# Performance work log

Hardware: AMD Instinct MI355X
Metric: run time of the kernel (lower is better)

Reference implementation:

```python
import jax, jax.numpy as jnp
import numpy as np

NUM_FEATURES = 128
NUM_FILTERS = 128

def setup_inputs() -> dict:
    key = jax.random.key(0)
    k1, k2, k3, k4, k5 = jax.random.split(key, 5)
    B, N, F = 4, 2048, NUM_FEATURES
    x = jax.random.normal(k1, (B, N, F), dtype=jnp.float32)
    A = jax.random.normal(k2, (B, N, N), dtype=jnp.float32)
    # Conv1D(num_filters, kernel_size=1, use_bias=False) == per-node linear F -> filters
    W = jax.random.normal(k3, (F, NUM_FILTERS), dtype=jnp.float32) * (1.0 / np.sqrt(F))
    # self.a: Conv1D(1, kernel_size=1) with bias == linear filters -> 1 (shared for x_i and x_j)
    a_w = jax.random.normal(k4, (NUM_FILTERS, 1), dtype=jnp.float32) * (1.0 / np.sqrt(NUM_FILTERS))
    a_b = jax.random.normal(k5, (1,), dtype=jnp.float32) * 0.01
    bias = jnp.zeros((NUM_FILTERS,), dtype=jnp.float32)
    return {"x": x, "A": A, "W": W, "a_w": a_w, "a_b": a_b, "bias": bias}

def reference(x, A, W, a_w, a_b, bias):
    # project features: [B,N,F] @ [F,Ff] -> [B,N,Ff]
    h = jnp.einsum('bnf,fg->bng', x, W)
    # shared attention projection (x_i and x_j use the same layer): [B,N,1]
    s = jnp.einsum('bng,go->bno', h, a_w) + a_b
    # additive scores s_i + s_j^T -> [B,N,N]
    e = s + jnp.swapaxes(s, 1, 2)
    e = jnp.where(e >= 0, e, 0.2 * e)  # LeakyReLU(0.2)
    attn = jax.nn.softmax(e + A, axis=-1)
    out = jnp.einsum('bij,bjg->big', attn, h) + bias
    return out
```

## Files before the change

kernel.cpp:

```cpp
#include <hip/hip_runtime.h>
#include <hip/hip_bf16.h>
#include <stdint.h>

#define BB 4
#define NN 2048
#define FF 128

typedef __attribute__((ext_vector_type(8))) short bf16x8;
typedef __attribute__((ext_vector_type(4))) float f32x4;

__device__ inline unsigned pk_bf16(float a, float b) {
    union { float f; unsigned u; } x, y;
    x.f = a; y.f = b;
    unsigned xu = x.u + (0x7fffu + ((x.u >> 16) & 1u));
    unsigned yu = y.u + (0x7fffu + ((y.u >> 16) & 1u));
    return (xu >> 16) | (yu & 0xffff0000u);
}

#define XT_P 136
#define WT_P 136

__global__ __launch_bounds__(256) void k1_proj(
    const float* __restrict__ x, const float* __restrict__ W,
    const float* __restrict__ a_w, const float* __restrict__ a_b,
    uint16_t* __restrict__ Ht, float* __restrict__ s_out)
{
    __shared__ uint16_t xt[16 * XT_P];
    __shared__ uint16_t Wt[128 * WT_P];
    __shared__ float sredw[4 * 16];

    const int t = threadIdx.x;
    const int w = t >> 6, l = t & 63;
    const int m16 = l & 15, q = l >> 4;
    const int b = blockIdx.x >> 7;
    const int n0 = (blockIdx.x & 127) << 4;

    const int c4 = (t & 31) * 4, kh = (t >> 5) * 16;
    float4 wr0[8], wr1[8];
    #pragma unroll
    for (int kk = 0; kk < 8; ++kk) {
        const int k = kh + 2 * kk;
        wr0[kk] = *(const float4*)(W + (size_t)k * 128 + c4);
        wr1[kk] = *(const float4*)(W + (size_t)(k + 1) * 128 + c4);
    }
    {
        const int row = t >> 4, c0 = (t & 15) * 8;
        const float* xr = x + ((size_t)(b * NN + n0 + row)) * FF + c0;
        const float4 v0 = *(const float4*)xr;
        const float4 v1 = *(const float4*)(xr + 4);
        unsigned* dst = (unsigned*)(xt + row * XT_P + c0);
        dst[0] = pk_bf16(v0.x, v0.y); dst[1] = pk_bf16(v0.z, v0.w);
        dst[2] = pk_bf16(v1.x, v1.y); dst[3] = pk_bf16(v1.z, v1.w);
    }
    #pragma unroll
    for (int kk = 0; kk < 8; ++kk) {
        const int k = kh + 2 * kk;
        *(unsigned*)(Wt + (c4 + 0) * WT_P + k) = pk_bf16(wr0[kk].x, wr1[kk].x);
        *(unsigned*)(Wt + (c4 + 1) * WT_P + k) = pk_bf16(wr0[kk].y, wr1[kk].y);
        *(unsigned*)(Wt + (c4 + 2) * WT_P + k) = pk_bf16(wr0[kk].z, wr1[kk].z);
        *(unsigned*)(Wt + (c4 + 3) * WT_P + k) = pk_bf16(wr0[kk].w, wr1[kk].w);
    }
    const int g0 = (2 * w) * 16 + m16, g1 = (2 * w + 1) * 16 + m16;
    const float aw0 = a_w[g0], aw1 = a_w[g1];
    __syncthreads();

    f32x4 acc0 = {}, acc1 = {};
    bf16x8 af[4];
    #pragma unroll
    for (int dk = 0; dk < 4; ++dk)
        af[dk] = *(const bf16x8*)(xt + m16 * XT_P + dk * 32 + q * 8);
    #pragma unroll
    for (int dk = 0; dk < 4; ++dk) {
        bf16x8 b0 = *(const bf16x8*)(Wt + g0 * WT_P + dk * 32 + q * 8);
        bf16x8 b1 = *(const bf16x8*)(Wt + g1 * WT_P + dk * 32 + q * 8);
        acc0 = __builtin_amdgcn_mfma_f32_16x16x32_bf16(af[dk], b0, acc0, 0, 0, 0);
        acc1 = __builtin_amdgcn_mfma_f32_16x16x32_bf16(af[dk], b1, acc1, 0, 0, 0);
    }

    float sp[4];
    #pragma unroll
    for (int r = 0; r < 4; ++r) sp[r] = acc0[r] * aw0 + acc1[r] * aw1;
    #pragma unroll
    for (int off = 1; off < 16; off <<= 1)
        #pragma unroll
        for (int r = 0; r < 4; ++r) sp[r] += __shfl_xor(sp[r], off, 64);
    if (m16 == 0) {
        #pragma unroll
        for (int r = 0; r < 4; ++r) sredw[w * 16 + q * 4 + r] = sp[r];
    }
    {
        uint2 o0 = { pk_bf16(acc0[0], acc0[1]), pk_bf16(acc0[2], acc0[3]) };
        uint2 o1 = { pk_bf16(acc1[0], acc1[1]), pk_bf16(acc1[2], acc1[3]) };
        *(uint2*)(Ht + ((size_t)(b * 128 + g0)) * NN + n0 + q * 4) = o0;
        *(uint2*)(Ht + ((size_t)(b * 128 + g1)) * NN + n0 + q * 4) = o1;
    }
    __syncthreads();
    if (t < 16)
        s_out[b * NN + n0 + t] = sredw[t] + sredw[16 + t] + sredw[32 + t] + sredw[48 + t] + a_b[0];
}

#define JS 8
#define IRND 8
#define P_RW 132
#define O_RW 36

__global__ __launch_bounds__(256, 2) void k2_attn(
    const float* __restrict__ A, const uint16_t* __restrict__ Ht,
    const float* __restrict__ s, uint16_t* __restrict__ po,
    float* __restrict__ prs)
{
    __shared__ unsigned Pbuf[2][16 * P_RW];
    __shared__ float    Osc[4][16 * O_RW];
    __shared__ float    rsw[2][4][16];

    const int t = threadIdx.x;
    const int w = t >> 6, l = t & 63;
    const int m16 = l & 15, q = l >> 4;

    const int bx = blockIdx.x;
    const int b  = bx & 3;
    const int js = (bx >> 2) & 7;
    const int is = bx >> 5;
    const int j0 = js * 256;
    const int ibase = is * 128;

    const float* sb = s + b * NN;
    const float* Ab = A + (size_t)b * NN * NN;
    const uint16_t* Hb = Ht + (size_t)b * FF * NN;

    const int jc0 = j0 + w * 32 + q * 8;
    const int jc1 = j0 + (w + 4) * 32 + q * 8;

    float4 sj00 = *(const float4*)(sb + jc0);
    float4 sj01 = *(const float4*)(sb + jc0 + 4);
    float4 sj10 = *(const float4*)(sb + jc1);
    float4 sj11 = *(const float4*)(sb + jc1 + 4);

    bf16x8 hf0[8], hf1[8];
    #pragma unroll
    for (int ks = 0; ks < 8; ++ks) {
        const int jj = j0 + ks * 32 + q * 8;
        hf0[ks] = *(const bf16x8*)(Hb + (size_t)(w * 32 + m16) * NN + jj);
        hf1[ks] = *(const bf16x8*)(Hb + (size_t)(w * 32 + 16 + m16) * NN + jj);
    }

    const float* Ar = Ab + (size_t)(ibase + m16) * NN;
    float4 a00 = *(const float4*)(Ar + jc0);
    float4 a01 = *(const float4*)(Ar + jc0 + 4);
    float4 a10 = *(const float4*)(Ar + jc1);
    float4 a11 = *(const float4*)(Ar + jc1 + 4);
    float si = sb[ibase + m16];

    const size_t slice = (size_t)(js * BB + b);

    #pragma unroll
    for (int r = 0; r < IRND; ++r) {
        const int i0r = ibase + r * 16;
        const int i0n = ibase + ((r + 1) & (IRND - 1)) * 16;
        const int par = r & 1;

        const float* An = Ab + (size_t)(i0n + m16) * NN;
        float4 n00 = *(const float4*)(An + jc0);
        float4 n01 = *(const float4*)(An + jc0 + 4);
        float4 n10 = *(const float4*)(An + jc1);
        float4 n11 = *(const float4*)(An + jc1 + 4);
        const float sin_ = sb[i0n + m16];

        const float svv[16] = {sj00.x,sj00.y,sj00.z,sj00.w, sj01.x,sj01.y,sj01.z,sj01.w,
                               sj10.x,sj10.y,sj10.z,sj10.w, sj11.x,sj11.y,sj11.z,sj11.w};
        const float avv[16] = {a00.x,a00.y,a00.z,a00.w, a01.x,a01.y,a01.z,a01.w,
                               a10.x,a10.y,a10.z,a10.w, a11.x,a11.y,a11.z,a11.w};
        float pv[16]; float rs = 0.f;
        #pragma unroll
        for (int j = 0; j < 16; ++j) {
            float e = si + svv[j];
            e = fmaxf(e, 0.2f * e);
            pv[j] = __expf(e + avv[j]);
            rs += pv[j];
        }
        union { unsigned u[4]; uint4 v4; } fa0, fa1;
        #pragma unroll
        for (int j = 0; j < 4; ++j) {
            fa0.u[j] = pk_bf16(pv[2 * j], pv[2 * j + 1]);
            fa1.u[j] = pk_bf16(pv[8 + 2 * j], pv[9 + 2 * j]);
        }
        *(uint4*)&Pbuf[par][m16 * P_RW + (w * 4 + q) * 4]        = fa0.v4;
        *(uint4*)&Pbuf[par][m16 * P_RW + (w * 4 + q + 16) * 4]   = fa1.v4;

        rs += __shfl_xor(rs, 16, 64);
        rs += __shfl_xor(rs, 32, 64);
        if (q == 0) rsw[par][w][m16] = rs;

        asm volatile("s_waitcnt lgkmcnt(0)\n\ts_barrier" ::: "memory");

        bf16x8 pa[8];
        #pragma unroll
        for (int ks = 0; ks < 8; ++ks)
            pa[ks] = *(const bf16x8*)&Pbuf[par][m16 * P_RW + ks * 16 + q * 4];

        f32x4 acc0 = {0.f, 0.f, 0.f, 0.f}, acc1 = {0.f, 0.f, 0.f, 0.f};
        #pragma unroll
        for (int ks = 0; ks < 8; ++ks) {
            acc0 = __builtin_amdgcn_mfma_f32_16x16x32_bf16(pa[ks], hf0[ks], acc0, 0, 0, 0);
            acc1 = __builtin_amdgcn_mfma_f32_16x16x32_bf16(pa[ks], hf1[ks], acc1, 0, 0, 0);
        }

        #pragma unroll
        for (int rr = 0; rr < 4; ++rr) {
            Osc[w][(q * 4 + rr) * O_RW + m16]      = acc0[rr];
            Osc[w][(q * 4 + rr) * O_RW + 16 + m16] = acc1[rr];
        }
        {
            const int row = l >> 2, c0 = (l & 3) * 8;
            const float4 u0 = *(const float4*)&Osc[w][row * O_RW + c0];
            const float4 u1 = *(const float4*)&Osc[w][row * O_RW + c0 + 4];
            uint4 ov = { pk_bf16(u0.x, u0.y), pk_bf16(u0.z, u0.w),
                         pk_bf16(u1.x, u1.y), pk_bf16(u1.z, u1.w) };
            *(uint4*)(po + ((slice * NN + i0r + row) * FF + w * 32 + c0)) = ov;
            if (t < 16)
                prs[slice * NN + i0r + t] = rsw[par][0][t] + rsw[par][1][t]
                                          + rsw[par][2][t] + rsw[par][3][t];
        }

        a00 = n00; a01 = n01; a10 = n10; a11 = n11; si = sin_;
    }
}

__global__ __launch_bounds__(256) void k3_red(
    const uint16_t* __restrict__ po, const float* __restrict__ prs,
    const float* __restrict__ bias, float* __restrict__ out)
{
    const int gid = blockIdx.x * 256 + threadIdx.x;
    const int g8 = (gid & 15) * 8;
    const int i = (gid >> 4) & (NN - 1);
    const int b = gid >> 15;

    float v[8] = {0.f,0.f,0.f,0.f,0.f,0.f,0.f,0.f};
    float rsum = 0.f;
    #pragma unroll
    for (int js = 0; js < JS; ++js) {
        const size_t base = (size_t)(js * BB + b) * NN + i;
        const uint4 pv_ = *(const uint4*)(po + base * FF + g8);
        const unsigned uu[4] = {pv_.x, pv_.y, pv_.z, pv_.w};
        #pragma unroll
        for (int k = 0; k < 4; ++k) {
            union { unsigned u; float f; } lo, hi;
            lo.u = uu[k] << 16;
            hi.u = uu[k] & 0xffff0000u;
            v[2 * k]     += lo.f;
            v[2 * k + 1] += hi.f;
        }
        rsum += prs[base];
    }
    const float inv = 1.0f / rsum;
    const float4 b0 = *(const float4*)(bias + g8);
    const float4 b1 = *(const float4*)(bias + g8 + 4);
    float4 o0 = { v[0]*inv + b0.x, v[1]*inv + b0.y, v[2]*inv + b0.z, v[3]*inv + b0.w };
    float4 o1 = { v[4]*inv + b1.x, v[5]*inv + b1.y, v[6]*inv + b1.z, v[7]*inv + b1.w };
    float* op = out + ((size_t)(b * NN + i)) * FF + g8;
    *(float4*)op = o0;
    *(float4*)(op + 4) = o1;
}

extern "C" void kernel_launch(void* const* d_in, const int* in_sizes, int n_in,
                              void* d_out, int out_size, void* d_ws, size_t ws_size,
                              hipStream_t stream) {
    const float* x    = (const float*)d_in[0];
    const float* A    = (const float*)d_in[1];
    const float* W    = (const float*)d_in[2];
    const float* a_w  = (const float*)d_in[3];
    const float* a_b  = (const float*)d_in[4];
    const float* bias = (const float*)d_in[5];
    float* out = (float*)d_out;

    char* ws = (char*)d_ws;
    uint16_t* Ht = (uint16_t*)ws;
    float* s = (float*)(ws + 2 * 1024 * 1024);
    uint16_t* po = (uint16_t*)(ws + 2 * 1024 * 1024 + 65536);
    float* prs = (float*)(ws + 2 * 1024 * 1024 + 65536 + (size_t)JS * BB * NN * FF * 2);

    k1_proj<<<BB * (NN / 16), 256, 0, stream>>>(x, W, a_w, a_b, Ht, s);
    k2_attn<<<JS * 16 * BB, 256, 0, stream>>>(A, Ht, s, po, prs);
    k3_red<<<(BB * NN * FF) / (256 * 8), 256, 0, stream>>>(po, prs, bias, out);
}
```

Baseline: 120.3 us.

## Compute attention probabilities per wave in registers, dropping LDS exchange and barrier

Each wave now computes exp-scores for its 16 rows across all 256 j columns itself and feeds them straight into the MFMA A operand. This removes the shared-memory P buffer, the per-round barrier and the cross-wave row-sum exchange. In exchange every wave loads the full A tile and s vector and repeats the exp work, about four times the per-block A load traffic and transcendental work. It also holds 64 more registers for the prefetched A fragments, and the round loop is no longer fully unrolled.

New measurement: 145.8 us. 21.2% more time.

```diff
diff --git a/kernel.cpp b/kernel.cpp
--- a/kernel.cpp
+++ b/kernel.cpp
@@ -101,7 +101,6 @@
 
 #define JS 8
 #define IRND 8
-#define P_RW 132
 #define O_RW 36
 
 __global__ __launch_bounds__(256, 2) void k2_attn(
@@ -109,9 +108,7 @@
     const float* __restrict__ s, uint16_t* __restrict__ po,
     float* __restrict__ prs)
 {
-    __shared__ unsigned Pbuf[2][16 * P_RW];
-    __shared__ float    Osc[4][16 * O_RW];
-    __shared__ float    rsw[2][4][16];
+    __shared__ float Osc[4][16 * O_RW];
 
     const int t = threadIdx.x;
     const int w = t >> 6, l = t & 63;
@@ -128,14 +125,6 @@
     const float* Ab = A + (size_t)b * NN * NN;
     const uint16_t* Hb = Ht + (size_t)b * FF * NN;
 
-    const int jc0 = j0 + w * 32 + q * 8;
-    const int jc1 = j0 + (w + 4) * 32 + q * 8;
-
-    float4 sj00 = *(const float4*)(sb + jc0);
-    float4 sj01 = *(const float4*)(sb + jc0 + 4);
-    float4 sj10 = *(const float4*)(sb + jc1);
-    float4 sj11 = *(const float4*)(sb + jc1 + 4);
-
     bf16x8 hf0[8], hf1[8];
     #pragma unroll
     for (int ks = 0; ks < 8; ++ks) {
@@ -144,66 +133,59 @@
         hf1[ks] = *(const bf16x8*)(Hb + (size_t)(w * 32 + 16 + m16) * NN + jj);
     }
 
-    const float* Ar = Ab + (size_t)(ibase + m16) * NN;
-    float4 a00 = *(const float4*)(Ar + jc0);
-    float4 a01 = *(const float4*)(Ar + jc0 + 4);
-    float4 a10 = *(const float4*)(Ar + jc1);
-    float4 a11 = *(const float4*)(Ar + jc1 + 4);
-    float si = sb[ibase + m16];
+    const float* sjp = sb + j0 + q * 8;
+
+    float4 af[16];
+    {
+        const float* Ar0 = Ab + (size_t)(ibase + m16) * NN + j0 + q * 8;
+        #pragma unroll
+        for (int ks = 0; ks < 8; ++ks) {
+            af[2 * ks]     = *(const float4*)(Ar0 + ks * 32);
+            af[2 * ks + 1] = *(const float4*)(Ar0 + ks * 32 + 4);
+        }
+    }
 
     const size_t slice = (size_t)(js * BB + b);
 
-    #pragma unroll
     for (int r = 0; r < IRND; ++r) {
         const int i0r = ibase + r * 16;
         const int i0n = ibase + ((r + 1) & (IRND - 1)) * 16;
-        const int par = r & 1;
-
-        const float* An = Ab + (size_t)(i0n + m16) * NN;
-        float4 n00 = *(const float4*)(An + jc0);
-        float4 n01 = *(const float4*)(An + jc0 + 4);
-        float4 n10 = *(const float4*)(An + jc1);
-        float4 n11 = *(const float4*)(An + jc1 + 4);
-        const float sin_ = sb[i0n + m16];
-
-        const float svv[16] = {sj00.x,sj00.y,sj00.z,sj00.w, sj01.x,sj01.y,sj01.z,sj01.w,
-                               sj10.x,sj10.y,sj10.z,sj10.w, sj11.x,sj11.y,sj11.z,sj11.w};
-        const float avv[16] = {a00.x,a00.y,a00.z,a00.w, a01.x,a01.y,a01.z,a01.w,
-                               a10.x,a10.y,a10.z,a10.w, a11.x,a11.y,a11.z,a11.w};
-        float pv[16]; float rs = 0.f;
-        #pragma unroll
-        for (int j = 0; j < 16; ++j) {
-            float e = si + svv[j];
-            e = fmaxf(e, 0.2f * e);
-            pv[j] = __expf(e + avv[j]);
-            rs += pv[j];
-        }
-        union { unsigned u[4]; uint4 v4; } fa0, fa1;
-        #pragma unroll
-        for (int j = 0; j < 4; ++j) {
-            fa0.u[j] = pk_bf16(pv[2 * j], pv[2 * j + 1]);
-            fa1.u[j] = pk_bf16(pv[8 + 2 * j], pv[9 + 2 * j]);
-        }
-        *(uint4*)&Pbuf[par][m16 * P_RW + (w * 4 + q) * 4]        = fa0.v4;
-        *(uint4*)&Pbuf[par][m16 * P_RW + (w * 4 + q + 16) * 4]   = fa1.v4;
+        const float* An = Ab + (size_t)(i0n + m16) * NN + j0 + q * 8;
+        const float si = sb[i0r + m16];
+
+        f32x4 acc0 = {0.f, 0.f, 0.f, 0.f}, acc1 = {0.f, 0.f, 0.f, 0.f};
+        float rs = 0.f;
+
+        #pragma unroll
+        for (int ks = 0; ks < 8; ++ks) {
+            const float4 a0 = af[2 * ks], a1 = af[2 * ks + 1];
+            af[2 * ks]     = *(const float4*)(An + ks * 32);
+            af[2 * ks + 1] = *(const float4*)(An + ks * 32 + 4);
+            const float4 s0 = *(const float4*)(sjp + ks * 32);
+            const float4 s1 = *(const float4*)(sjp + ks * 32 + 4);
+
+            const float av[8] = {a0.x,a0.y,a0.z,a0.w, a1.x,a1.y,a1.z,a1.w};
+            const float sv[8] = {s0.x,s0.y,s0.z,s0.w, s1.x,s1.y,s1.z,s1.w};
+            float p8[8];
+            #pragma unroll
+            for (int j = 0; j < 8; ++j) {
+                float e = si + sv[j];
+                e = fmaxf(e, 0.2f * e);
+                p8[j] = __expf(e + av[j]);
+                rs += p8[j];
+            }
+            union { unsigned u[4]; bf16x8 v; } pa;
+            #pragma unroll
+            for (int j = 0; j < 4; ++j)
+                pa.u[j] = pk_bf16(p8[2 * j], p8[2 * j + 1]);
+
+            acc0 = __builtin_amdgcn_mfma_f32_16x16x32_bf16(pa.v, hf0[ks], acc0, 0, 0, 0);
+            acc1 = __builtin_amdgcn_mfma_f32_16x16x32_bf16(pa.v, hf1[ks], acc1, 0, 0, 0);
+        }
 
         rs += __shfl_xor(rs, 16, 64);
         rs += __shfl_xor(rs, 32, 64);
-        if (q == 0) rsw[par][w][m16] = rs;
-
-        asm volatile("s_waitcnt lgkmcnt(0)\n\ts_barrier" ::: "memory");
-
-        bf16x8 pa[8];
-        #pragma unroll
-        for (int ks = 0; ks < 8; ++ks)
-            pa[ks] = *(const bf16x8*)&Pbuf[par][m16 * P_RW + ks * 16 + q * 4];
-
-        f32x4 acc0 = {0.f, 0.f, 0.f, 0.f}, acc1 = {0.f, 0.f, 0.f, 0.f};
-        #pragma unroll
-        for (int ks = 0; ks < 8; ++ks) {
-            acc0 = __builtin_amdgcn_mfma_f32_16x16x32_bf16(pa[ks], hf0[ks], acc0, 0, 0, 0);
-            acc1 = __builtin_amdgcn_mfma_f32_16x16x32_bf16(pa[ks], hf1[ks], acc1, 0, 0, 0);
-        }
+        if (t < 16) prs[slice * NN + i0r + t] = rs;
 
         #pragma unroll
         for (int rr = 0; rr < 4; ++rr) {
@@ -217,12 +199,7 @@
             uint4 ov = { pk_bf16(u0.x, u0.y), pk_bf16(u0.z, u0.w),
                          pk_bf16(u1.x, u1.y), pk_bf16(u1.z, u1.w) };
             *(uint4*)(po + ((slice * NN + i0r + row) * FF + w * 32 + c0)) = ov;
-            if (t < 16)
-                prs[slice * NN + i0r + t] = rsw[par][0][t] + rsw[par][1][t]
-                                          + rsw[par][2][t] + rsw[par][3][t];
-        }
-
-        a00 = n00; a01 = n01; a10 = n10; a11 = n11; si = sin_;
+        }
     }
 }
 
```

## Software-pipeline softmax weight computation one round ahead of MFMA in attention kernel

Applied to the files above, without the earlier changes.

Restructures the attention loop so the exp/LeakyReLU computation and bf16 packing for round r+1 happen before the MFMAs of round r, writing into the alternate LDS buffer. A prologue computes round 0, and A rows are prefetched two rounds ahead. The row-sum scratch gets a third slot to avoid a write-after-read hazard, and a barrier is added at the end of each iteration. The aim is to overlap VALU/transcendental work with matrix-core work and hide A load latency, at the cost of more live registers and a prefetch that may limit occupancy.

Result: no change. 122.6 us (+1.9%).

```diff
diff --git a/kernel.cpp b/kernel.cpp
--- a/kernel.cpp
+++ b/kernel.cpp
@@ -111,7 +111,7 @@
 {
     __shared__ unsigned Pbuf[2][16 * P_RW];
     __shared__ float    Osc[4][16 * O_RW];
-    __shared__ float    rsw[2][4][16];
+    __shared__ float    rsw[3][4][16];
 
     const int t = threadIdx.x;
     const int w = t >> 6, l = t & 63;
@@ -144,28 +144,17 @@
         hf1[ks] = *(const bf16x8*)(Hb + (size_t)(w * 32 + 16 + m16) * NN + jj);
     }
 
-    const float* Ar = Ab + (size_t)(ibase + m16) * NN;
-    float4 a00 = *(const float4*)(Ar + jc0);
-    float4 a01 = *(const float4*)(Ar + jc0 + 4);
-    float4 a10 = *(const float4*)(Ar + jc1);
-    float4 a11 = *(const float4*)(Ar + jc1 + 4);
-    float si = sb[ibase + m16];
-
-    const size_t slice = (size_t)(js * BB + b);
-
-    #pragma unroll
-    for (int r = 0; r < IRND; ++r) {
-        const int i0r = ibase + r * 16;
-        const int i0n = ibase + ((r + 1) & (IRND - 1)) * 16;
-        const int par = r & 1;
-
-        const float* An = Ab + (size_t)(i0n + m16) * NN;
-        float4 n00 = *(const float4*)(An + jc0);
-        float4 n01 = *(const float4*)(An + jc0 + 4);
-        float4 n10 = *(const float4*)(An + jc1);
-        float4 n11 = *(const float4*)(An + jc1 + 4);
-        const float sin_ = sb[i0n + m16];
-
+    float si_all[IRND];
+    #pragma unroll
+    for (int rr = 0; rr < IRND; ++rr) si_all[rr] = sb[ibase + rr * 16 + m16];
+
+    const float* Ar0 = Ab + (size_t)(ibase + m16) * NN;
+    float4 a00 = *(const float4*)(Ar0 + jc0);
+    float4 a01 = *(const float4*)(Ar0 + jc0 + 4);
+    float4 a10 = *(const float4*)(Ar0 + jc1);
+    float4 a11 = *(const float4*)(Ar0 + jc1 + 4);
+
+    {
         const float svv[16] = {sj00.x,sj00.y,sj00.z,sj00.w, sj01.x,sj01.y,sj01.z,sj01.w,
                                sj10.x,sj10.y,sj10.z,sj10.w, sj11.x,sj11.y,sj11.z,sj11.w};
         const float avv[16] = {a00.x,a00.y,a00.z,a00.w, a01.x,a01.y,a01.z,a01.w,
@@ -173,7 +162,7 @@
         float pv[16]; float rs = 0.f;
         #pragma unroll
         for (int j = 0; j < 16; ++j) {
-            float e = si + svv[j];
+            float e = si_all[0] + svv[j];
             e = fmaxf(e, 0.2f * e);
             pv[j] = __expf(e + avv[j]);
             rs += pv[j];
@@ -184,19 +173,65 @@
             fa0.u[j] = pk_bf16(pv[2 * j], pv[2 * j + 1]);
             fa1.u[j] = pk_bf16(pv[8 + 2 * j], pv[9 + 2 * j]);
         }
-        *(uint4*)&Pbuf[par][m16 * P_RW + (w * 4 + q) * 4]        = fa0.v4;
-        *(uint4*)&Pbuf[par][m16 * P_RW + (w * 4 + q + 16) * 4]   = fa1.v4;
-
+        *(uint4*)&Pbuf[0][m16 * P_RW + (w * 4 + q) * 4]      = fa0.v4;
+        *(uint4*)&Pbuf[0][m16 * P_RW + (w * 4 + q + 16) * 4] = fa1.v4;
         rs += __shfl_xor(rs, 16, 64);
         rs += __shfl_xor(rs, 32, 64);
-        if (q == 0) rsw[par][w][m16] = rs;
-
-        asm volatile("s_waitcnt lgkmcnt(0)\n\ts_barrier" ::: "memory");
+        if (q == 0) rsw[0][w][m16] = rs;
+    }
+    {
+        const float* An = Ab + (size_t)(ibase + 16 + m16) * NN;
+        a00 = *(const float4*)(An + jc0);
+        a01 = *(const float4*)(An + jc0 + 4);
+        a10 = *(const float4*)(An + jc1);
+        a11 = *(const float4*)(An + jc1 + 4);
+    }
+    asm volatile("s_waitcnt lgkmcnt(0)\n\ts_barrier" ::: "memory");
+
+    const size_t slice = (size_t)(js * BB + b);
+
+    #pragma unroll
+    for (int r = 0; r < IRND; ++r) {
+        const int i0r = ibase + r * 16;
+        const int par = r & 1;
 
         bf16x8 pa[8];
         #pragma unroll
         for (int ks = 0; ks < 8; ++ks)
             pa[ks] = *(const bf16x8*)&Pbuf[par][m16 * P_RW + ks * 16 + q * 4];
+
+        if (r < IRND - 1) {
+            const float svv[16] = {sj00.x,sj00.y,sj00.z,sj00.w, sj01.x,sj01.y,sj01.z,sj01.w,
+                                   sj10.x,sj10.y,sj10.z,sj10.w, sj11.x,sj11.y,sj11.z,sj11.w};
+            const float avv[16] = {a00.x,a00.y,a00.z,a00.w, a01.x,a01.y,a01.z,a01.w,
+                                   a10.x,a10.y,a10.z,a10.w, a11.x,a11.y,a11.z,a11.w};
+            float pv[16]; float rs = 0.f;
+            #pragma unroll
+            for (int j = 0; j < 16; ++j) {
+                float e = si_all[r + 1] + svv[j];
+                e = fmaxf(e, 0.2f * e);
+                pv[j] = __expf(e + avv[j]);
+                rs += pv[j];
+            }
+            union { unsigned u[4]; uint4 v4; } fa0, fa1;
+            #pragma unroll
+            for (int j = 0; j < 4; ++j) {
+                fa0.u[j] = pk_bf16(pv[2 * j], pv[2 * j + 1]);
+                fa1.u[j] = pk_bf16(pv[8 + 2 * j], pv[9 + 2 * j]);
+            }
+            *(uint4*)&Pbuf[par ^ 1][m16 * P_RW + (w * 4 + q) * 4]      = fa0.v4;
+            *(uint4*)&Pbuf[par ^ 1][m16 * P_RW + (w * 4 + q + 16) * 4] = fa1.v4;
+            rs += __shfl_xor(rs, 16, 64);
+            rs += __shfl_xor(rs, 32, 64);
+            if (q == 0) rsw[(r + 1) % 3][w][m16] = rs;
+
+            const int i2 = ibase + ((r + 2) & (IRND - 1)) * 16;
+            const float* An = Ab + (size_t)(i2 + m16) * NN;
+            a00 = *(const float4*)(An + jc0);
+            a01 = *(const float4*)(An + jc0 + 4);
+            a10 = *(const float4*)(An + jc1);
+            a11 = *(const float4*)(An + jc1 + 4);
+        }
 
         f32x4 acc0 = {0.f, 0.f, 0.f, 0.f}, acc1 = {0.f, 0.f, 0.f, 0.f};
         #pragma unroll
@@ -218,11 +253,11 @@
                          pk_bf16(u1.x, u1.y), pk_bf16(u1.z, u1.w) };
             *(uint4*)(po + ((slice * NN + i0r + row) * FF + w * 32 + c0)) = ov;
             if (t < 16)
-                prs[slice * NN + i0r + t] = rsw[par][0][t] + rsw[par][1][t]
-                                          + rsw[par][2][t] + rsw[par][3][t];
-        }
-
-        a00 = n00; a01 = n01; a10 = n10; a11 = n11; si = sin_;
+                prs[slice * NN + i0r + t] = rsw[r % 3][0][t] + rsw[r % 3][1][t]
+                                          + rsw[r % 3][2][t] + rsw[r % 3][3][t];
+        }
+
+        asm volatile("s_waitcnt lgkmcnt(0)\n\ts_barrier" ::: "memory");
     }
 }
 
```
